# Kernel tuning notes

Hardware: AMD Instinct MI355X
Metric: run time of the kernel (lower is better)

## Reference

```python
import jax, jax.numpy as jnp
import numpy as np

B, T, C = 2, 2048, 2048
N_HEADS, N_KV_HEADS = 16, 4
HEAD_DIM = C // N_HEADS  # 128
NUM_GROUPS = N_HEADS // N_KV_HEADS  # 4


def setup_inputs() -> dict:
    key = jax.random.key(0)
    ks = jax.random.split(key, 5)
    s = 1.0 / np.sqrt(C)
    return {
        "x": jax.random.normal(ks[0], (B, T, C), dtype=jnp.float32),
        "Wq": jax.random.normal(ks[1], (C, N_HEADS * HEAD_DIM), dtype=jnp.float32) * s,
        "Wk": jax.random.normal(ks[2], (C, N_KV_HEADS * HEAD_DIM), dtype=jnp.float32) * s,
        "Wv": jax.random.normal(ks[3], (C, N_KV_HEADS * HEAD_DIM), dtype=jnp.float32) * s,
        "Wo": jax.random.normal(ks[4], (C, C), dtype=jnp.float32) * s,
    }


def _rope_tables(seq_len, head_dim, dtype):
    theta = 1.0 / (10000.0 ** (jnp.arange(0, head_dim, 2, dtype=jnp.float32) / head_dim))
    freqs = jnp.arange(seq_len, dtype=jnp.float32)[:, None] * theta[None, :]  # [T, hd/2]
    cos = jnp.concatenate([jnp.cos(freqs), jnp.cos(freqs)], axis=-1)  # [T, hd]
    sin = jnp.concatenate([jnp.sin(freqs), jnp.sin(freqs)], axis=-1)
    return cos.astype(dtype), sin.astype(dtype)


def _rotate_half(x):
    x1, x2 = jnp.split(x, 2, axis=-1)
    return jnp.concatenate([-x2, x1], axis=-1)


def reference(x, Wq, Wk, Wv, Wo):
    b, t, c = x.shape
    q = (x @ Wq).reshape(b, t, N_HEADS, HEAD_DIM).transpose(0, 2, 1, 3)      # [B,H,T,hd]
    k = (x @ Wk).reshape(b, t, N_KV_HEADS, HEAD_DIM).transpose(0, 2, 1, 3)   # [B,Hkv,T,hd]
    v = (x @ Wv).reshape(b, t, N_KV_HEADS, HEAD_DIM).transpose(0, 2, 1, 3)

    cos, sin = _rope_tables(t, HEAD_DIM, x.dtype)  # [T,hd]
    cos = cos[None, None]  # [1,1,T,hd]
    sin = sin[None, None]
    q = q * cos + _rotate_half(q) * sin
    k = k * cos + _rotate_half(k) * sin

    # GQA: expand kv heads (repeat_interleave along head dim)
    k = jnp.repeat(k, NUM_GROUPS, axis=1)  # [B,H,T,hd]
    v = jnp.repeat(v, NUM_GROUPS, axis=1)

    scale = 1.0 / jnp.sqrt(jnp.asarray(HEAD_DIM, dtype=x.dtype))
    scores = jnp.einsum("bhqd,bhkd->bhqk", q, k) * scale  # [B,H,T,T]
    causal = jnp.tril(jnp.ones((t, t), dtype=bool))
    scores = jnp.where(causal[None, None], scores, jnp.asarray(-jnp.inf, dtype=scores.dtype))
    attn = jax.nn.softmax(scores, axis=-1)
    out = jnp.einsum("bhqk,bhkd->bhqd", attn, v)  # [B,H,T,hd]
    out = out.transpose(0, 2, 1, 3).reshape(b, t, c)
    return out @ Wo
```

## Files before the change

### kernel.cpp

```cpp
#include <hip/hip_runtime.h>
#include <hip/hip_bf16.h>
#include <math.h>

typedef __hip_bfloat16 bf16;
typedef __attribute__((ext_vector_type(8))) short bf16x8;
typedef __attribute__((ext_vector_type(4))) float floatx4;

__device__ __forceinline__ void async_copy16(const bf16* g, bf16* l) {
    __builtin_amdgcn_global_load_lds(
        (__attribute__((address_space(1))) void*)(void*)g,
        (__attribute__((address_space(3))) void*)(void*)l,
        16, 0, 0);
}

__global__ __launch_bounds__(256) void cast_f32_bf16(const float* __restrict__ in,
                                                     bf16* __restrict__ out, int n4) {
    int i = blockIdx.x * 256 + threadIdx.x;
    if (i >= n4) return;
    float4 v = ((const float4*)in)[i];
    union { ushort4 u; bf16 b[4]; } o;
    o.b[0] = __float2bfloat16(v.x);
    o.b[1] = __float2bfloat16(v.y);
    o.b[2] = __float2bfloat16(v.z);
    o.b[3] = __float2bfloat16(v.w);
    ((ushort4*)out)[i] = o.u;
}

__global__ __launch_bounds__(256) void cast_transpose(const float* __restrict__ in,
                                                      bf16* __restrict__ out, int K, int N) {
    __shared__ float tile[32][33];
    int nb = blockIdx.x * 32, kb = blockIdx.y * 32;
    for (int j = threadIdx.y; j < 32; j += 8)
        tile[j][threadIdx.x] = in[(size_t)(kb + j) * N + nb + threadIdx.x];
    __syncthreads();
    for (int j = threadIdx.y; j < 32; j += 8)
        out[(size_t)(nb + j) * K + kb + threadIdx.x] = __float2bfloat16(tile[threadIdx.x][j]);
}

template <bool OUTF32>
__global__ __launch_bounds__(256) void gemm_bt(const bf16* __restrict__ A,
                                               const bf16* __restrict__ Bt,
                                               void* __restrict__ Cout,
                                               int M, int N, int K) {
    __shared__ bf16 As[128 * 32];
    __shared__ bf16 Bs[128 * 32];
    const int tid = threadIdx.x;
    const int wave = tid >> 6, lane = tid & 63;
    const int c = lane & 15, quad = lane >> 4;
    const int wm = wave >> 1, wn = wave & 1;
    const int mBase = blockIdx.y * 128, nBase = blockIdx.x * 128;

    const int sRow = lane >> 2;
    const int sCol = ((lane & 3) ^ ((lane >> 3) & 3)) << 3;
    const int rdOff = (quad ^ ((c >> 1) & 3)) << 3;
    const bf16* gA = A + (size_t)(mBase + wave * 32 + sRow) * K + sCol;
    const bf16* gB = Bt + (size_t)(nBase + wave * 32 + sRow) * K + sCol;
    bf16* lA = As + wave * 1024;
    bf16* lB = Bs + wave * 1024;

    floatx4 acc[4][4];
#pragma unroll
    for (int mt = 0; mt < 4; mt++)
#pragma unroll
        for (int nt = 0; nt < 4; nt++) acc[mt][nt] = (floatx4){0.f, 0.f, 0.f, 0.f};

    for (int k0 = 0; k0 < K; k0 += 32) {
        async_copy16(gA + k0, lA);
        async_copy16(gA + k0 + 16 * K, lA + 512);
        async_copy16(gB + k0, lB);
        async_copy16(gB + k0 + 16 * K, lB + 512);
        __syncthreads();
        bf16x8 af[4], bfr[4];
#pragma unroll
        for (int mt = 0; mt < 4; mt++)
            af[mt] = *(const bf16x8*)(As + (wm * 64 + mt * 16 + c) * 32 + rdOff);
#pragma unroll
        for (int nt = 0; nt < 4; nt++)
            bfr[nt] = *(const bf16x8*)(Bs + (wn * 64 + nt * 16 + c) * 32 + rdOff);
#pragma unroll
        for (int mt = 0; mt < 4; mt++)
#pragma unroll
            for (int nt = 0; nt < 4; nt++)
                acc[mt][nt] = __builtin_amdgcn_mfma_f32_16x16x32_bf16(af[mt], bfr[nt],
                                                                      acc[mt][nt], 0, 0, 0);
        __syncthreads();
    }
#pragma unroll
    for (int mt = 0; mt < 4; mt++)
#pragma unroll
        for (int nt = 0; nt < 4; nt++)
#pragma unroll
            for (int r = 0; r < 4; r++) {
                int row = mBase + wm * 64 + mt * 16 + quad * 4 + r;
                int col = nBase + wn * 64 + nt * 16 + c;
                if (OUTF32)
                    ((float*)Cout)[(size_t)row * N + col] = acc[mt][nt][r];
                else
                    ((bf16*)Cout)[(size_t)row * N + col] = __float2bfloat16(acc[mt][nt][r]);
            }
}

__global__ __launch_bounds__(256) void rope_kernel(bf16* __restrict__ X, int heads, int rowStride) {
    int idx = blockIdx.x * 256 + threadIdx.x;
    int d = idx & 63;
    int h = (idx >> 6) % heads;
    int row = idx / (heads * 64);
    int t = row & 2047;
    float theta = exp2f(-(float)d * 0.20762050593045827f);
    float ang = (float)t * theta;
    float sv, cv;
    __sincosf(ang, &sv, &cv);
    bf16* p = X + (size_t)row * rowStride + h * 128 + d;
    float x1 = __bfloat162float(p[0]);
    float x2 = __bfloat162float(p[64]);
    p[0]  = __float2bfloat16(x1 * cv - x2 * sv);
    p[64] = __float2bfloat16(x2 * cv + x1 * sv);
}

__global__ __launch_bounds__(256) void vtrans(const bf16* __restrict__ QKV,
                                              bf16* __restrict__ Vtg) {
    __shared__ bf16 tile[32][34];
    const int bh = blockIdx.z;
    const int b = bh >> 2, kvh = bh & 3;
    const int t0 = blockIdx.x * 32, d0 = blockIdx.y * 32;
    const bf16* src = QKV + (size_t)b * 2048 * 3072 + 2560 + kvh * 128;
    for (int j = threadIdx.y; j < 32; j += 8)
        tile[j][threadIdx.x] = src[(size_t)(t0 + j) * 3072 + d0 + threadIdx.x];
    __syncthreads();
    bf16* dst = Vtg + (size_t)bh * 128 * 2048;
    for (int j = threadIdx.y; j < 32; j += 8)
        dst[(size_t)(d0 + j) * 2048 + t0 + threadIdx.x] = tile[threadIdx.x][j];
}

__global__ __launch_bounds__(256, 4) void flash_attn5(const bf16* __restrict__ QKV,
                                                      const bf16* __restrict__ Vtg,
                                                      bf16* __restrict__ Slot0,
                                                      bf16* __restrict__ Slot1,
                                                      float* __restrict__ Ls) {
    const int T = 2048, STR = 3072;
    __shared__ bf16 Ks[4 * 64 * 32];
    __shared__ bf16 Vs[2 * 128 * 32];
    __shared__ bf16 Pl[4][16 * 40];
    const int b = blockIdx.z, h = blockIdx.y;
    const int pj = blockIdx.x >> 1, s = blockIdx.x & 1;
    const int kvh = h >> 2;
    const int tid = threadIdx.x, wave = tid >> 6, lane = tid & 63;
    const int c = lane & 15, quad = lane >> 4;
    const float C2 = 0.12751541717525597f;

    const bf16* Kg = QKV + (size_t)b * T * STR + 2048 + kvh * 128;
    const bf16* Vg = Vtg + (size_t)(b * 4 + kvh) * 128 * 2048;
    const int srow = tid >> 2;
    const int xcol = ((tid & 3) ^ ((tid >> 3) & 3)) << 3;
    const int koff = (quad ^ ((c >> 1) & 3)) << 3;
    bf16* PlW = &Pl[wave][0];
    const int qa = 31 - pj;

    auto run_part = [&](int qtile, int ktlo, int kthi, bf16* slot, int lsSlot) {
        const int q0 = qtile * 64;
        bf16x8 qf[4];
        {
            const bf16* qp = QKV + ((size_t)b * T + q0 + wave * 16 + c) * STR + h * 128 + quad * 8;
#pragma unroll
            for (int ks = 0; ks < 4; ks++) qf[ks] = *(const bf16x8*)(qp + ks * 32);
            const float t = (float)(q0 + wave * 16 + c);
#pragma unroll
            for (int ks = 0; ks < 2; ks++)
#pragma unroll
                for (int j = 0; j < 8; j++) {
                    int d = ks * 32 + quad * 8 + j;
                    float theta = exp2f((float)d * -0.20762050593045827f);
                    float sv, cv;
                    __sincosf(t * theta, &sv, &cv);
                    float lo = __bfloat162float(((const bf16*)&qf[ks])[j]);
                    float hi = __bfloat162float(((const bf16*)&qf[ks + 2])[j]);
                    ((bf16*)&qf[ks])[j]     = __float2bfloat16((lo * cv - hi * sv) * C2);
                    ((bf16*)&qf[ks + 2])[j] = __float2bfloat16((hi * cv + lo * sv) * C2);
                }
        }
        floatx4 accO[8];
#pragma unroll
        for (int nt = 0; nt < 8; nt++) accO[nt] = (floatx4){0.f, 0.f, 0.f, 0.f};
        float lrow[4] = {0.f, 0.f, 0.f, 0.f};

        for (int kt = ktlo; kt < kthi; kt++) {
            const int kt0 = kt * 64;
#pragma unroll
            for (int it = 0; it < 4; it++) {
                async_copy16(Kg + (size_t)(kt0 + srow) * STR + it * 32 + xcol,
                             Ks + it * 2048 + wave * 512);
                async_copy16(Vg + (size_t)((it & 1) * 64 + srow) * 2048 + kt0 + (it >> 1) * 32 + xcol,
                             Vs + it * 2048 + wave * 512);
            }
            __syncthreads();
            floatx4 sf[4];
#pragma unroll
            for (int nt = 0; nt < 4; nt++) sf[nt] = (floatx4){0.f, 0.f, 0.f, 0.f};
#pragma unroll
            for (int ks = 0; ks < 4; ks++)
#pragma unroll
                for (int nt = 0; nt < 4; nt++) {
                    bf16x8 kf = *(const bf16x8*)(Ks + ks * 2048 + (nt * 16 + c) * 32 + koff);
                    sf[nt] = __builtin_amdgcn_mfma_f32_16x16x32_bf16(qf[ks], kf, sf[nt], 0, 0, 0);
                }
            const int lim = (kt == qtile) ? (wave * 16 + quad * 4) : 1000;
#pragma unroll
            for (int kc = 0; kc < 2; kc++) {
#pragma unroll
                for (int nt2 = 0; nt2 < 2; nt2++) {
                    const int nt = kc * 2 + nt2;
#pragma unroll
                    for (int r = 0; r < 4; r++) {
                        float p = exp2f(sf[nt][r]);
                        if (nt * 16 + c > lim + r) p = 0.f;
                        lrow[r] += p;
                        PlW[(quad * 4 + r) * 40 + nt2 * 16 + c] = __float2bfloat16(p);
                    }
                }
                asm volatile("s_waitcnt lgkmcnt(0)" ::: "memory");
                bf16x8 pf = *(const bf16x8*)(PlW + c * 40 + quad * 8);
#pragma unroll
                for (int nt = 0; nt < 8; nt++) {
                    bf16x8 vf = *(const bf16x8*)(Vs + kc * 4096 + (nt * 16 + c) * 32 + koff);
                    accO[nt] = __builtin_amdgcn_mfma_f32_16x16x32_bf16(pf, vf, accO[nt], 0, 0, 0);
                }
                asm volatile("" ::: "memory");
            }
            __syncthreads();
        }
        float sred[4];
#pragma unroll
        for (int r = 0; r < 4; r++) {
            float v = lrow[r];
            v += __shfl_xor(v, 1);
            v += __shfl_xor(v, 2);
            v += __shfl_xor(v, 4);
            v += __shfl_xor(v, 8);
            sred[r] = v;
        }
        if (c == 0) {
#pragma unroll
            for (int r = 0; r < 4; r++)
                Ls[(size_t)lsSlot * 65536 + ((size_t)(b * 16 + h) * 32 + qtile) * 64
                   + wave * 16 + quad * 4 + r] = sred[r];
        }
        const size_t orow = (size_t)b * T + q0 + wave * 16 + quad * 4;
#pragma unroll
        for (int nt = 0; nt < 8; nt++)
#pragma unroll
            for (int r = 0; r < 4; r++)
                slot[(orow + r) * 2048 + h * 128 + nt * 16 + c] =
                    __float2bfloat16(accO[nt][r]);
    };

    if (s == 0) {
        run_part(qa, 0, 17, Slot0, 0);
    } else {
        run_part(qa, 17, 32 - pj, Slot1, 1);
        run_part(pj, 0, pj + 1, Slot0, 0);
    }
}

__global__ __launch_bounds__(256) void attn_merge(bf16* __restrict__ AO,
                                                  const bf16* __restrict__ P1,
                                                  const float* __restrict__ Ls) {
    int i = blockIdx.x * 256 + threadIdx.x;
    int row = i >> 8;
    int cg = (i & 255) << 3;
    int b = row >> 11, t = row & 2047;
    int qtile = t >> 6;
    int h = cg >> 7;
    size_t off = (size_t)row * 2048 + cg;
    size_t li = ((size_t)(b * 16 + h) * 32 + qtile) * 64 + (t & 63);
    bf16x8 a0 = *(const bf16x8*)(AO + off);
    float l = Ls[li];
    float acc[8];
#pragma unroll
    for (int j = 0; j < 8; j++) acc[j] = __bfloat162float(((const bf16*)&a0)[j]);
    if (qtile >= 16) {
        bf16x8 a1 = *(const bf16x8*)(P1 + off);
        l += Ls[65536 + li];
#pragma unroll
        for (int j = 0; j < 8; j++) acc[j] += __bfloat162float(((const bf16*)&a1)[j]);
    }
    float inv = 1.0f / l;
    bf16x8 o;
#pragma unroll
    for (int j = 0; j < 8; j++) ((bf16*)&o)[j] = __float2bfloat16(acc[j] * inv);
    *(bf16x8*)(AO + off) = o;
}

extern "C" void kernel_launch(void* const* d_in, const int* in_sizes, int n_in,
                              void* d_out, int out_size, void* d_ws, size_t ws_size,
                              hipStream_t stream) {
    const float* x  = (const float*)d_in[0];
    const float* Wq = (const float*)d_in[1];
    const float* Wk = (const float*)d_in[2];
    const float* Wv = (const float*)d_in[3];
    const float* Wo = (const float*)d_in[4];

    char* ws = (char*)d_ws;
    bf16* xb   = (bf16*)(ws);
    bf16* Vtg  = (bf16*)(ws);
    bf16* Slt1 = (bf16*)(ws + 4194304);
    float* Ls  = (float*)(ws + 20971520);
    bf16* Wt   = (bf16*)(ws + 16777216);
    bf16* Wot  = (bf16*)(ws + 29360128);
    bf16* QKV  = (bf16*)(ws + 37748736);
    bf16* AO   = (bf16*)(ws + 62914560);

    cast_f32_bf16<<<8192, 256, 0, stream>>>(x, xb, 2097152);
    cast_transpose<<<dim3(64, 64), dim3(32, 8), 0, stream>>>(Wq, Wt, 2048, 2048);
    cast_transpose<<<dim3(16, 64), dim3(32, 8), 0, stream>>>(Wk, Wt + 2048 * 2048, 2048, 512);
    cast_transpose<<<dim3(16, 64), dim3(32, 8), 0, stream>>>(Wv, Wt + 2560 * 2048, 2048, 512);
    cast_transpose<<<dim3(64, 64), dim3(32, 8), 0, stream>>>(Wo, Wot, 2048, 2048);

    gemm_bt<false><<<dim3(24, 32), 256, 0, stream>>>(xb, Wt, QKV, 4096, 3072, 2048);

    rope_kernel<<<4096, 256, 0, stream>>>(QKV + 2048, 4, 3072);

    vtrans<<<dim3(64, 4, 8), dim3(32, 8), 0, stream>>>(QKV, Vtg);

    flash_attn5<<<dim3(32, 16, 2), 256, 0, stream>>>(QKV, Vtg, AO, Slt1, Ls);

    attn_merge<<<4096, 256, 0, stream>>>(AO, Slt1, Ls);

    gemm_bt<true><<<dim3(16, 32), 256, 0, stream>>>(AO, Wot, d_out, 4096, 2048, 2048);
}
```

Before: 326.1 us.

## Transpose attention MFMA operands, specialise diagonal tile, split-K output GEMM with atomics

The flash attention kernel swaps MFMA operand order so each lane holds a full query row. That turns the row-sum reduction into two shuffles, lets P be written to LDS as swizzled 4-wide vectors without the explicit waitcnt, and allows vectorised output stores. The causal mask moves into a compile-time diagonal-only tile variant, so off-diagonal tiles skip the mask compare. The output projection becomes a split-K GEMM with two K halves accumulated into a zeroed fp32 output via atomic adds, doubling grid parallelism at the cost of a memset and atomic traffic.

```diff
diff --git a/kernel.cpp b/kernel.cpp
--- a/kernel.cpp
+++ b/kernel.cpp
@@ -1,9 +1,11 @@
 #include <hip/hip_runtime.h>
 #include <hip/hip_bf16.h>
 #include <math.h>
+#include <utility>
 
 typedef __hip_bfloat16 bf16;
 typedef __attribute__((ext_vector_type(8))) short bf16x8;
+typedef __attribute__((ext_vector_type(4))) short bf16x4;
 typedef __attribute__((ext_vector_type(4))) float floatx4;
 
 __device__ __forceinline__ void async_copy16(const bf16* g, bf16* l) {
@@ -37,10 +39,9 @@
         out[(size_t)(nb + j) * K + kb + threadIdx.x] = __float2bfloat16(tile[threadIdx.x][j]);
 }
 
-template <bool OUTF32>
 __global__ __launch_bounds__(256) void gemm_bt(const bf16* __restrict__ A,
                                                const bf16* __restrict__ Bt,
-                                               void* __restrict__ Cout,
+                                               bf16* __restrict__ Cout,
                                                int M, int N, int K) {
     __shared__ bf16 As[128 * 32];
     __shared__ bf16 Bs[128 * 32];
@@ -93,10 +94,67 @@
             for (int r = 0; r < 4; r++) {
                 int row = mBase + wm * 64 + mt * 16 + quad * 4 + r;
                 int col = nBase + wn * 64 + nt * 16 + c;
-                if (OUTF32)
-                    ((float*)Cout)[(size_t)row * N + col] = acc[mt][nt][r];
-                else
-                    ((bf16*)Cout)[(size_t)row * N + col] = __float2bfloat16(acc[mt][nt][r]);
+                Cout[(size_t)row * N + col] = __float2bfloat16(acc[mt][nt][r]);
+            }
+}
+
+__global__ __launch_bounds__(256) void gemm_bt_sk(const bf16* __restrict__ A,
+                                                  const bf16* __restrict__ Bt,
+                                                  float* __restrict__ Cout,
+                                                  int M, int N, int K) {
+    __shared__ bf16 As[128 * 32];
+    __shared__ bf16 Bs[128 * 32];
+    const int tid = threadIdx.x;
+    const int wave = tid >> 6, lane = tid & 63;
+    const int c = lane & 15, quad = lane >> 4;
+    const int wm = wave >> 1, wn = wave & 1;
+    const int mBase = blockIdx.y * 128, nBase = blockIdx.x * 128;
+    const int kz = blockIdx.z * 1024;
+
+    const int sRow = lane >> 2;
+    const int sCol = ((lane & 3) ^ ((lane >> 3) & 3)) << 3;
+    const int rdOff = (quad ^ ((c >> 1) & 3)) << 3;
+    const bf16* gA = A + (size_t)(mBase + wave * 32 + sRow) * K + sCol;
+    const bf16* gB = Bt + (size_t)(nBase + wave * 32 + sRow) * K + sCol;
+    bf16* lA = As + wave * 1024;
+    bf16* lB = Bs + wave * 1024;
+
+    floatx4 acc[4][4];
+#pragma unroll
+    for (int mt = 0; mt < 4; mt++)
+#pragma unroll
+        for (int nt = 0; nt < 4; nt++) acc[mt][nt] = (floatx4){0.f, 0.f, 0.f, 0.f};
+
+    for (int k0 = kz; k0 < kz + 1024; k0 += 32) {
+        async_copy16(gA + k0, lA);
+        async_copy16(gA + k0 + 16 * K, lA + 512);
+        async_copy16(gB + k0, lB);
+        async_copy16(gB + k0 + 16 * K, lB + 512);
+        __syncthreads();
+        bf16x8 af[4], bfr[4];
+#pragma unroll
+        for (int mt = 0; mt < 4; mt++)
+            af[mt] = *(const bf16x8*)(As + (wm * 64 + mt * 16 + c) * 32 + rdOff);
+#pragma unroll
+        for (int nt = 0; nt < 4; nt++)
+            bfr[nt] = *(const bf16x8*)(Bs + (wn * 64 + nt * 16 + c) * 32 + rdOff);
+#pragma unroll
+        for (int mt = 0; mt < 4; mt++)
+#pragma unroll
+            for (int nt = 0; nt < 4; nt++)
+                acc[mt][nt] = __builtin_amdgcn_mfma_f32_16x16x32_bf16(af[mt], bfr[nt],
+                                                                      acc[mt][nt], 0, 0, 0);
+        __syncthreads();
+    }
+#pragma unroll
+    for (int mt = 0; mt < 4; mt++)
+#pragma unroll
+        for (int nt = 0; nt < 4; nt++)
+#pragma unroll
+            for (int r = 0; r < 4; r++) {
+                int row = mBase + wm * 64 + mt * 16 + quad * 4 + r;
+                int col = nBase + wn * 64 + nt * 16 + c;
+                unsafeAtomicAdd(&Cout[(size_t)row * N + col], acc[mt][nt][r]);
             }
 }
 
@@ -132,7 +190,7 @@
         dst[(size_t)(d0 + j) * 2048 + t0 + threadIdx.x] = tile[threadIdx.x][j];
 }
 
-__global__ __launch_bounds__(256, 4) void flash_attn5(const bf16* __restrict__ QKV,
+__global__ __launch_bounds__(256, 4) void flash_attn6(const bf16* __restrict__ QKV,
                                                       const bf16* __restrict__ Vtg,
                                                       bf16* __restrict__ Slot0,
                                                       bf16* __restrict__ Slot1,
@@ -140,7 +198,7 @@
     const int T = 2048, STR = 3072;
     __shared__ bf16 Ks[4 * 64 * 32];
     __shared__ bf16 Vs[2 * 128 * 32];
-    __shared__ bf16 Pl[4][16 * 40];
+    __shared__ bf16 Pl[4][16 * 64];
     const int b = blockIdx.z, h = blockIdx.y;
     const int pj = blockIdx.x >> 1, s = blockIdx.x & 1;
     const int kvh = h >> 2;
@@ -154,6 +212,7 @@
     const int xcol = ((tid & 3) ^ ((tid >> 3) & 3)) << 3;
     const int koff = (quad ^ ((c >> 1) & 3)) << 3;
     bf16* PlW = &Pl[wave][0];
+    const int pwBase = c * 64 + (quad & 1) * 4;
     const int qa = 31 - pj;
 
     auto run_part = [&](int qtile, int ktlo, int kthi, bf16* slot, int lsSlot) {
@@ -181,10 +240,10 @@
         floatx4 accO[8];
 #pragma unroll
         for (int nt = 0; nt < 8; nt++) accO[nt] = (floatx4){0.f, 0.f, 0.f, 0.f};
-        float lrow[4] = {0.f, 0.f, 0.f, 0.f};
-
-        for (int kt = ktlo; kt < kthi; kt++) {
-            const int kt0 = kt * 64;
+        float lrow = 0.f;
+
+        auto tile = [&](int kt0, auto DIAGC) {
+            constexpr bool DIAG = decltype(DIAGC)::value;
 #pragma unroll
             for (int it = 0; it < 4; it++) {
                 async_copy16(Kg + (size_t)(kt0 + srow) * STR + it * 32 + xcol,
@@ -201,56 +260,53 @@
 #pragma unroll
                 for (int nt = 0; nt < 4; nt++) {
                     bf16x8 kf = *(const bf16x8*)(Ks + ks * 2048 + (nt * 16 + c) * 32 + koff);
-                    sf[nt] = __builtin_amdgcn_mfma_f32_16x16x32_bf16(qf[ks], kf, sf[nt], 0, 0, 0);
+                    sf[nt] = __builtin_amdgcn_mfma_f32_16x16x32_bf16(kf, qf[ks], sf[nt], 0, 0, 0);
                 }
-            const int lim = (kt == qtile) ? (wave * 16 + quad * 4) : 1000;
+#pragma unroll
+            for (int nt = 0; nt < 4; nt++) {
+                bf16x4 pk;
+#pragma unroll
+                for (int r = 0; r < 4; r++) {
+                    float p = exp2f(sf[nt][r]);
+                    if (DIAG)
+                        if (nt * 16 + quad * 4 + r > wave * 16 + c) p = 0.f;
+                    lrow += p;
+                    ((bf16*)&pk)[r] = __float2bfloat16(p);
+                }
+                *(bf16x4*)(PlW + pwBase + (((nt * 2 + (quad >> 1)) ^ (c & 7)) << 3)) = pk;
+            }
 #pragma unroll
             for (int kc = 0; kc < 2; kc++) {
-#pragma unroll
-                for (int nt2 = 0; nt2 < 2; nt2++) {
-                    const int nt = kc * 2 + nt2;
-#pragma unroll
-                    for (int r = 0; r < 4; r++) {
-                        float p = exp2f(sf[nt][r]);
-                        if (nt * 16 + c > lim + r) p = 0.f;
-                        lrow[r] += p;
-                        PlW[(quad * 4 + r) * 40 + nt2 * 16 + c] = __float2bfloat16(p);
-                    }
-                }
-                asm volatile("s_waitcnt lgkmcnt(0)" ::: "memory");
-                bf16x8 pf = *(const bf16x8*)(PlW + c * 40 + quad * 8);
+                bf16x8 pf = *(const bf16x8*)(PlW + c * 64 + ((((kc << 2) + quad) ^ (c & 7)) << 3));
 #pragma unroll
                 for (int nt = 0; nt < 8; nt++) {
                     bf16x8 vf = *(const bf16x8*)(Vs + kc * 4096 + (nt * 16 + c) * 32 + koff);
-                    accO[nt] = __builtin_amdgcn_mfma_f32_16x16x32_bf16(pf, vf, accO[nt], 0, 0, 0);
+                    accO[nt] = __builtin_amdgcn_mfma_f32_16x16x32_bf16(vf, pf, accO[nt], 0, 0, 0);
                 }
-                asm volatile("" ::: "memory");
             }
             __syncthreads();
+        };
+
+        const int ndiag = (kthi > qtile) ? qtile : kthi;
+        for (int kt = ktlo; kt < ndiag; kt++)
+            tile(kt * 64, std::integral_constant<bool, false>{});
+        if (kthi > qtile)
+            tile(qtile * 64, std::integral_constant<bool, true>{});
+
+        float sred = lrow;
+        sred += __shfl_xor(sred, 16);
+        sred += __shfl_xor(sred, 32);
+        if (quad == 0)
+            Ls[(size_t)lsSlot * 65536 + ((size_t)(b * 16 + h) * 32 + qtile) * 64
+               + wave * 16 + c] = sred;
+        bf16* orow = slot + (size_t)(b * T + q0 + wave * 16 + c) * 2048 + h * 128 + quad * 4;
+#pragma unroll
+        for (int nt = 0; nt < 8; nt++) {
+            bf16x4 o;
+#pragma unroll
+            for (int r = 0; r < 4; r++) ((bf16*)&o)[r] = __float2bfloat16(accO[nt][r]);
+            *(bf16x4*)(orow + nt * 16) = o;
         }
-        float sred[4];
-#pragma unroll
-        for (int r = 0; r < 4; r++) {
-            float v = lrow[r];
-            v += __shfl_xor(v, 1);
-            v += __shfl_xor(v, 2);
-            v += __shfl_xor(v, 4);
-            v += __shfl_xor(v, 8);
-            sred[r] = v;
-        }
-        if (c == 0) {
-#pragma unroll
-            for (int r = 0; r < 4; r++)
-                Ls[(size_t)lsSlot * 65536 + ((size_t)(b * 16 + h) * 32 + qtile) * 64
-                   + wave * 16 + quad * 4 + r] = sred[r];
-        }
-        const size_t orow = (size_t)b * T + q0 + wave * 16 + quad * 4;
-#pragma unroll
-        for (int nt = 0; nt < 8; nt++)
-#pragma unroll
-            for (int r = 0; r < 4; r++)
-                slot[(orow + r) * 2048 + h * 128 + nt * 16 + c] =
-                    __float2bfloat16(accO[nt][r]);
     };
 
     if (s == 0) {
@@ -309,21 +365,23 @@
     bf16* QKV  = (bf16*)(ws + 37748736);
     bf16* AO   = (bf16*)(ws + 62914560);
 
+    hipMemsetAsync(d_out, 0, (size_t)out_size * 4, stream);
+
     cast_f32_bf16<<<8192, 256, 0, stream>>>(x, xb, 2097152);
     cast_transpose<<<dim3(64, 64), dim3(32, 8), 0, stream>>>(Wq, Wt, 2048, 2048);
     cast_transpose<<<dim3(16, 64), dim3(32, 8), 0, stream>>>(Wk, Wt + 2048 * 2048, 2048, 512);
     cast_transpose<<<dim3(16, 64), dim3(32, 8), 0, stream>>>(Wv, Wt + 2560 * 2048, 2048, 512);
     cast_transpose<<<dim3(64, 64), dim3(32, 8), 0, stream>>>(Wo, Wot, 2048, 2048);
 
-    gemm_bt<false><<<dim3(24, 32), 256, 0, stream>>>(xb, Wt, QKV, 4096, 3072, 2048);
+    gemm_bt<<<dim3(24, 32), 256, 0, stream>>>(xb, Wt, QKV, 4096, 3072, 2048);
 
     rope_kernel<<<4096, 256, 0, stream>>>(QKV + 2048, 4, 3072);
 
     vtrans<<<dim3(64, 4, 8), dim3(32, 8), 0, stream>>>(QKV, Vtg);
 
-    flash_attn5<<<dim3(32, 16, 2), 256, 0, stream>>>(QKV, Vtg, AO, Slt1, Ls);
+    flash_attn6<<<dim3(32, 16, 2), 256, 0, stream>>>(QKV, Vtg, AO, Slt1, Ls);
 
     attn_merge<<<4096, 256, 0, stream>>>(AO, Slt1, Ls);
 
-    gemm_bt<true><<<dim3(16, 32), 256, 0, stream>>>(AO, Wot, d_out, 4096, 2048, 2048);
-}
+    gemm_bt_sk<<<dim3(16, 32, 2), 256, 0, stream>>>(AO, Wot, (float*)d_out, 4096, 2048, 2048);
+}
```

Result: slower. 366.0 us (+12.2%).
